# Performance work log

Hardware: AMD Instinct MI355X
Metric: run time of the kernel (lower is better)

Reference implementation:

```python
import jax, jax.numpy as jnp
import numpy as np

DIM = 256
HEADS = 4
DIM_HEAD = 32
HIDDEN = HEADS * DIM_HEAD  # 128
SCALE = DIM_HEAD ** -0.5
EPS = 1e-5


def setup_inputs() -> dict:
    key = jax.random.key(0)
    k1, k2, k3, k4 = jax.random.split(key, 4)
    B, D, H, W = 4, 32, 32, 32
    x = jax.random.normal(k1, (B, DIM, D, H, W), dtype=jnp.float32)
    # 1x1x1 convs are just channel-mixing matrices
    w_qkv = jax.random.normal(k2, (HIDDEN * 3, DIM), dtype=jnp.float32) * (DIM ** -0.5)
    w_out = jax.random.normal(k3, (DIM, HIDDEN), dtype=jnp.float32) * (HIDDEN ** -0.5)
    bias_out = jax.random.normal(k4, (DIM,), dtype=jnp.float32) * 0.02
    gamma = jnp.ones((DIM,), dtype=jnp.float32)
    beta = jnp.zeros((DIM,), dtype=jnp.float32)
    return {"x": x, "w_qkv": w_qkv, "w_out": w_out, "bias_out": bias_out,
            "gamma": gamma, "beta": beta}


def reference(x, w_qkv, w_out, bias_out, gamma, beta):
    B, C, D, H, W = x.shape
    n = D * H * W
    # to_qkv: 1x1x1 conv, no bias -> channel matmul
    qkv = jnp.einsum('oc,bcdhw->bodhw', w_qkv, x)  # [B, 3*HIDDEN, D, H, W]
    qkv = qkv.reshape(B, 3, HEADS, DIM_HEAD, n)
    q, k, v = qkv[:, 0], qkv[:, 1], qkv[:, 2]       # each [B, HEADS, DIM_HEAD, n]
    q = jax.nn.softmax(q, axis=-2) * SCALE          # softmax over head-dim channels
    k = jax.nn.softmax(k, axis=-1)                  # softmax over spatial positions
    context = jnp.einsum('bhdn,bhen->bhde', k, v)   # [B, H, dh, dh]
    out = jnp.einsum('bhde,bhdn->bhen', context, q) # [B, H, dh, n]
    out = out.reshape(B, HIDDEN, D, H, W)
    # to_out conv (1x1x1, with bias)
    y = jnp.einsum('oc,bcdhw->bodhw', w_out, out) + bias_out[None, :, None, None, None]
    # LayerNorm3D over channel dim
    mean = jnp.mean(y, axis=1, keepdims=True)
    var = jnp.var(y, axis=1, keepdims=True)
    y = (y - mean) / jnp.sqrt(var + EPS)
    return y * gamma[None, :, None, None, None] + beta[None, :, None, None, None]
```

## Files before the change

### kernel.cpp

```cpp
#include <hip/hip_runtime.h>


typedef unsigned short us16;
typedef __attribute__((ext_vector_type(8))) short short8v;
typedef __attribute__((ext_vector_type(4))) float f32x4;

#define B_ 4
#define C_ 256
#define NO_ 384
#define N_ 32768
#define HEADS_ 4
#define DH_ 32
#define HID_ 128
#define SCALE_ 0.17677669529663687f
#define EPS_ 1e-5f
#define NCHUNK 128
#define CHN 256

__device__ __forceinline__ float bf2f(us16 u) {
    union { unsigned int i; float f; } v; v.i = ((unsigned int)u) << 16; return v.f;
}
__device__ __forceinline__ us16 f2bf(float f) {
    union { float f; unsigned int i; } v; v.f = f;
    unsigned int x = v.i;
    return (us16)((x + 0x7fffu + ((x >> 16) & 1u)) >> 16);
}
__device__ __forceinline__ bool f32_mode(const void* gamma) {
    return *reinterpret_cast<const unsigned int*>(gamma) == 0x3F800000u;
}
__device__ __forceinline__ float ldin(const void* p, size_t i, bool m) {
    return m ? reinterpret_cast<const float*>(p)[i]
             : bf2f(reinterpret_cast<const us16*>(p)[i]);
}
__device__ __forceinline__ void gload_lds16(const us16* g, us16* l) {
    __builtin_amdgcn_global_load_lds(
        (__attribute__((address_space(1))) void*)g,
        (__attribute__((address_space(3))) void*)l, 16, 0, 0);
}

__global__ __launch_bounds__(256) void k_cvtw(
    const void* __restrict__ w, const void* __restrict__ gamma, us16* __restrict__ wb)
{
    const bool m32 = f32_mode(gamma);
    int i4 = (blockIdx.x * 256 + threadIdx.x) * 4;
    if (m32) {
        float4 f = *reinterpret_cast<const float4*>(reinterpret_cast<const float*>(w) + i4);
        ushort4 u; u.x = f2bf(f.x); u.y = f2bf(f.y); u.z = f2bf(f.z); u.w = f2bf(f.w);
        *reinterpret_cast<ushort4*>(wb + i4) = u;
    } else {
        *reinterpret_cast<ushort4*>(wb + i4) =
            *reinterpret_cast<const ushort4*>(reinterpret_cast<const us16*>(w) + i4);
    }
}

__global__ __launch_bounds__(256) void k_tr(
    const void* __restrict__ x, const void* __restrict__ gamma, us16* __restrict__ xt)
{
    __shared__ us16 T[64][72];
    const bool m32 = f32_mode(gamma);
    const int t = threadIdx.x;
    const int n0 = blockIdx.x * 64;
    const int c0 = blockIdx.y * 64;
    const int b  = blockIdx.z;

    const int cb = (t >> 4) * 4;
    const int nb = (t & 15) * 4;
    float v[4][4];
#pragma unroll
    for (int i = 0; i < 4; i++) {
        size_t off = ((size_t)b * C_ + c0 + cb + i) * N_ + n0 + nb;
        if (m32) {
            float4 f = *reinterpret_cast<const float4*>(reinterpret_cast<const float*>(x) + off);
            v[i][0] = f.x; v[i][1] = f.y; v[i][2] = f.z; v[i][3] = f.w;
        } else {
            ushort4 u = *reinterpret_cast<const ushort4*>(reinterpret_cast<const us16*>(x) + off);
            v[i][0] = bf2f(u.x); v[i][1] = bf2f(u.y); v[i][2] = bf2f(u.z); v[i][3] = bf2f(u.w);
        }
    }
#pragma unroll
    for (int j = 0; j < 4; j++) {
        ushort4 u;
        u.x = f2bf(v[0][j]); u.y = f2bf(v[1][j]); u.z = f2bf(v[2][j]); u.w = f2bf(v[3][j]);
        *reinterpret_cast<ushort4*>(&T[nb + j][cb]) = u;
    }
    __syncthreads();
    const int n = t >> 2;
    const int ch = (t & 3) * 16;
    uint4 r0 = *reinterpret_cast<const uint4*>(&T[n][ch]);
    uint4 r1 = *reinterpret_cast<const uint4*>(&T[n][ch + 8]);
    us16* dst = xt + ((size_t)b * N_ + n0 + n) * C_ + c0 + ch;
    *reinterpret_cast<uint4*>(dst)     = r0;
    *reinterpret_cast<uint4*>(dst + 8) = r1;
}

__global__ __launch_bounds__(256) void k_qkv(
    const us16* __restrict__ xt, const us16* __restrict__ wb, us16* __restrict__ qkv)
{
    __shared__ us16 As[128][64];
    __shared__ us16 Bs[128][64];
    const int t  = threadIdx.x;
    const int bb = blockIdx.z;
    const int o0 = blockIdx.y * 128;
    const int p0 = blockIdx.x * 128;
    const int wid  = t >> 6;
    const int lane = t & 63;
    const int lr   = lane & 15;
    const int quad = lane >> 4;
    const int m0w = (wid >> 1) * 64;
    const int n0w = (wid & 1) * 64;

    const int srow = wid * 32 + (lane >> 3);
    const int scol = ((lane & 7) ^ (lane >> 3)) * 8;

    f32x4 acc[4][4];
#pragma unroll
    for (int mi = 0; mi < 4; mi++)
#pragma unroll
        for (int nj = 0; nj < 4; nj++) acc[mi][nj] = (f32x4){0.f, 0.f, 0.f, 0.f};

    for (int c0 = 0; c0 < C_; c0 += 64) {
        const us16* ag = wb + (size_t)(o0 + srow) * C_ + c0 + scol;
        const us16* bg = xt + ((size_t)bb * N_ + p0 + srow) * C_ + c0 + scol;
        us16* al = &As[wid * 32][0];
        us16* bl = &Bs[wid * 32][0];
#pragma unroll
        for (int j = 0; j < 4; j++) {
            gload_lds16(ag + (size_t)j * 8 * C_, al + j * 512);
            gload_lds16(bg + (size_t)j * 8 * C_, bl + j * 512);
        }
        __syncthreads();
        const int sw = (lr & 7) << 3;
#pragma unroll
        for (int k32 = 0; k32 < 64; k32 += 32) {
            short8v a[4], bfr[4];
            const int col = (k32 + quad * 8) ^ sw;
#pragma unroll
            for (int mi = 0; mi < 4; mi++)
                a[mi] = *reinterpret_cast<const short8v*>(&As[m0w + mi * 16 + lr][col]);
#pragma unroll
            for (int nj = 0; nj < 4; nj++)
                bfr[nj] = *reinterpret_cast<const short8v*>(&Bs[n0w + nj * 16 + lr][col]);
#pragma unroll
            for (int mi = 0; mi < 4; mi++)
#pragma unroll
                for (int nj = 0; nj < 4; nj++)
                    acc[mi][nj] = __builtin_amdgcn_mfma_f32_16x16x32_bf16(
                        a[mi], bfr[nj], acc[mi][nj], 0, 0, 0);
        }
        __syncthreads();
    }
#pragma unroll
    for (int mi = 0; mi < 4; mi++) {
#pragma unroll
        for (int rr = 0; rr < 4; rr++) {
            int o = o0 + m0w + mi * 16 + quad * 4 + rr;
            us16* cp = qkv + ((size_t)bb * NO_ + o) * N_ + p0 + n0w + lr;
#pragma unroll
            for (int nj = 0; nj < 4; nj++)
                cp[nj * 16] = f2bf(acc[mi][nj][rr]);
        }
    }
}

__global__ __launch_bounds__(256) void k_ctx_part(
    const us16* __restrict__ qkv, float* __restrict__ part)
{
    __shared__ us16 Kp[32][264];
    __shared__ us16 Vt[32][264];
    __shared__ float redM[4][32];
    __shared__ float redS[4][32];
    const int t = threadIdx.x;
    const int chunk = blockIdx.x;
    const int h = blockIdx.y;
    const int b = blockIdx.z;
    const int p0 = chunk * CHN;
    const us16* kbase = qkv + ((size_t)b * NO_ + HID_ + h * DH_) * N_;
    const us16* vbase = qkv + ((size_t)b * NO_ + 2 * HID_ + h * DH_) * N_;

    {
        const int r = t >> 3, c = (t & 7) * 32;
        const us16* kp = kbase + (size_t)r * N_ + p0 + c;
        const us16* vp = vbase + (size_t)r * N_ + p0 + c;
#pragma unroll
        for (int j = 0; j < 4; j++) {
            *reinterpret_cast<uint4*>(&Kp[r][c + j * 8]) = *reinterpret_cast<const uint4*>(kp + j * 8);
            *reinterpret_cast<uint4*>(&Vt[r][c + j * 8]) = *reinterpret_cast<const uint4*>(vp + j * 8);
        }
    }
    __syncthreads();

    const int d    = t & 31;
    const int seg  = t >> 5;
    const int wv   = t >> 6;
    const int lane = t & 63;
    const int lr   = lane & 15;
    const int quad = lane >> 4;

    float kv[32];
#pragma unroll
    for (int j = 0; j < 4; j++) {
        uint4 kq = *reinterpret_cast<const uint4*>(&Kp[d][seg * 32 + j * 8]);
        const us16* ks = reinterpret_cast<const us16*>(&kq);
#pragma unroll
        for (int u = 0; u < 8; u++) kv[j * 8 + u] = bf2f(ks[u]);
    }
    float m = -1e30f;
#pragma unroll
    for (int u = 0; u < 32; u++) m = fmaxf(m, kv[u]);
    m = fmaxf(m, __shfl_xor(m, 32));
    if (lane < 32) redM[wv][d] = m;
    __syncthreads();
    m = fmaxf(fmaxf(redM[0][d], redM[1][d]), fmaxf(redM[2][d], redM[3][d]));

    float s = 0.f;
    us16 pb[32];
#pragma unroll
    for (int u = 0; u < 32; u++) {
        float pv = __expf(kv[u] - m);
        s += pv;
        pb[u] = f2bf(pv);
    }
#pragma unroll
    for (int j = 0; j < 4; j++)
        *reinterpret_cast<uint4*>(&Kp[d][seg * 32 + j * 8]) =
            *reinterpret_cast<const uint4*>(&pb[j * 8]);
    s += __shfl_xor(s, 32);
    if (lane < 32) redS[wv][d] = s;
    __syncthreads();

    f32x4 acc[2][2];
#pragma unroll
    for (int mi = 0; mi < 2; mi++)
#pragma unroll
        for (int nj = 0; nj < 2; nj++) acc[mi][nj] = (f32x4){0.f, 0.f, 0.f, 0.f};
#pragma unroll
    for (int kk = 0; kk < 64; kk += 32) {
        const int k32 = wv * 64 + kk;
        short8v a[2], bfr[2];
#pragma unroll
        for (int mi = 0; mi < 2; mi++)
            a[mi] = *reinterpret_cast<const short8v*>(&Kp[mi * 16 + lr][k32 + quad * 8]);
#pragma unroll
        for (int nj = 0; nj < 2; nj++)
            bfr[nj] = *reinterpret_cast<const short8v*>(&Vt[nj * 16 + lr][k32 + quad * 8]);
#pragma unroll
        for (int mi = 0; mi < 2; mi++)
#pragma unroll
            for (int nj = 0; nj < 2; nj++)
                acc[mi][nj] = __builtin_amdgcn_mfma_f32_16x16x32_bf16(
                    a[mi], bfr[nj], acc[mi][nj], 0, 0, 0);
    }
    __syncthreads();

    float* wpart = reinterpret_cast<float*>(&Kp[0][0]);
#pragma unroll
    for (int mi = 0; mi < 2; mi++)
#pragma unroll
        for (int nj = 0; nj < 2; nj++)
#pragma unroll
            for (int rr = 0; rr < 4; rr++)
                wpart[wv * 1056 + (mi * 16 + quad * 4 + rr) * 33 + nj * 16 + lr] =
                    acc[mi][nj][rr];
    __syncthreads();

    const size_t base = (((size_t)(b * HEADS_ + h)) * NCHUNK + chunk) * 1088;
    {
        const int dd = t >> 3, e4 = (t & 7) * 4;
        float o0 = 0.f, o1 = 0.f, o2 = 0.f, o3 = 0.f;
#pragma unroll
        for (int w = 0; w < 4; w++) {
            const float* wp = wpart + w * 1056 + dd * 33 + e4;
            o0 += wp[0]; o1 += wp[1]; o2 += wp[2]; o3 += wp[3];
        }
        *reinterpret_cast<float4*>(&part[base + 64 + dd * 32 + e4]) =
            make_float4(o0, o1, o2, o3);
    }
    if (t < 32) {
        part[base + t] = m;
        part[base + 32 + t] = redS[0][t] + redS[1][t] + redS[2][t] + redS[3][t];
    }
}

__global__ __launch_bounds__(1024) void k_ctx_comb(
    const float* __restrict__ part, float* __restrict__ ctx)
{
    __shared__ float scale[NCHUNK][32];
    __shared__ float Mg[32];
    __shared__ float Sg[32];
    __shared__ float redm[32][32];
    __shared__ float reds[32][32];
    const int t = threadIdx.x;
    const int bh = blockIdx.x;
    const float* pb = part + (size_t)bh * NCHUNK * 1088;

    const int d = t & 31, g = t >> 5;
    float m = -1e30f;
    for (int c = g; c < NCHUNK; c += 32) m = fmaxf(m, pb[(size_t)c * 1088 + d]);
    redm[g][d] = m;
    __syncthreads();
    if (t < 32) {
        float mm = redm[0][t];
#pragma unroll
        for (int w = 1; w < 32; w++) mm = fmaxf(mm, redm[w][t]);
        Mg[t] = mm;
    }
    __syncthreads();
    float sacc = 0.f;
    for (int c = g; c < NCHUNK; c += 32) {
        float sc = __expf(pb[(size_t)c * 1088 + d] - Mg[d]);
        scale[c][d] = sc;
        sacc += sc * pb[(size_t)c * 1088 + 32 + d];
    }
    reds[g][d] = sacc;
    __syncthreads();
    if (t < 32) {
        float ss = 0.f;
#pragma unroll
        for (int w = 0; w < 32; w++) ss += reds[w][t];
        Sg[t] = 1.f / ss;
    }
    __syncthreads();

    const int dd = t >> 5;
    const int e  = t & 31;
    float a = 0.f;
    for (int c = 0; c < NCHUNK; c++)
        a += scale[c][dd] * pb[(size_t)c * 1088 + 64 + dd * 32 + e];
    ctx[((size_t)bh * DH_ + dd) * DH_ + e] = a * Sg[dd];
}

__global__ __launch_bounds__(256) void k_ctx(
    const us16* __restrict__ qkv, float* __restrict__ ctx)
{
    const int d = blockIdx.x;
    const int h = blockIdx.y;
    const int b = blockIdx.z;
    const int tid = threadIdx.x;
    const us16* krow  = qkv + ((size_t)b * NO_ + HID_ + h * DH_ + d) * N_;
    const us16* vbase = qkv + ((size_t)b * NO_ + 2 * HID_ + h * DH_) * N_;
    __shared__ float red[4];
    __shared__ float part[4][DH_];

    float m = -1e30f;
    for (int i = tid; i < N_; i += 256) m = fmaxf(m, bf2f(krow[i]));
#pragma unroll
    for (int off = 32; off; off >>= 1) m = fmaxf(m, __shfl_xor(m, off));
    if ((tid & 63) == 0) red[tid >> 6] = m;
    __syncthreads();
    m = fmaxf(fmaxf(red[0], red[1]), fmaxf(red[2], red[3]));
    __syncthreads();
    float s = 0.f;
    for (int i = tid; i < N_; i += 256) s += __expf(bf2f(krow[i]) - m);
#pragma unroll
    for (int off = 32; off; off >>= 1) s += __shfl_xor(s, off);
    if ((tid & 63) == 0) red[tid >> 6] = s;
    __syncthreads();
    s = red[0] + red[1] + red[2] + red[3];
    const float inv = 1.f / s;

    float acc[DH_];
#pragma unroll
    for (int e = 0; e < DH_; e++) acc[e] = 0.f;
    for (int i = tid; i < N_; i += 256) {
        float p = __expf(bf2f(krow[i]) - m) * inv;
#pragma unroll
        for (int e = 0; e < DH_; e++) acc[e] += p * bf2f(vbase[(size_t)e * N_ + i]);
    }
#pragma unroll
    for (int e = 0; e < DH_; e++) {
        float v2 = acc[e];
#pragma unroll
        for (int off = 32; off; off >>= 1) v2 += __shfl_xor(v2, off);
        acc[e] = v2;
    }
    const int wid = tid >> 6;
    if ((tid & 63) == 0) {
#pragma unroll
        for (int e = 0; e < DH_; e++) part[wid][e] = acc[e];
    }
    __syncthreads();
    if (tid < DH_) {
        float v2 = part[0][tid] + part[1][tid] + part[2][tid] + part[3][tid];
        ctx[(((size_t)b * HEADS_ + h) * DH_ + d) * DH_ + tid] = v2;
    }
}

__global__ __launch_bounds__(256) void k_w2(
    const void* __restrict__ wout, const float* __restrict__ ctx,
    const void* __restrict__ gamma, us16* __restrict__ w2b)
{
    const bool m32 = f32_mode(gamma);
    const int b = blockIdx.y;
    const int gid = blockIdx.x * 256 + (int)threadIdx.x;
    const int i = gid & 127;
    const int o = gid >> 7;
    const int h = i >> 5, d = i & 31;
    const float* cr = ctx + (((size_t)b * HEADS_ + h) * DH_ + d) * DH_;
    const size_t woff = (size_t)o * HID_ + h * DH_;
    float s = 0.f;
#pragma unroll
    for (int e = 0; e < DH_; e++) s += ldin(wout, woff + e, m32) * cr[e];
    w2b[((size_t)b * C_ + o) * HID_ + i] = f2bf(s);
}

__global__ __launch_bounds__(256) void k_out(
    const us16* __restrict__ qkv, const us16* __restrict__ w2b,
    const void* __restrict__ bias, const void* __restrict__ gamma,
    const void* __restrict__ beta, void* __restrict__ y)
{
    __shared__ us16 qsT[64][136];
    __shared__ float red1[4][64];
    __shared__ float red2[4][64];
    __shared__ float meanS[64];
    __shared__ float rstdS[64];
    const bool m32 = f32_mode(gamma);
    const int t  = threadIdx.x;
    const int bb = blockIdx.y;
    const int p0 = blockIdx.x * 64;

    {
        const int h = t >> 6, col = t & 63;
        const us16* qb = qkv + ((size_t)bb * NO_ + h * DH_) * N_ + p0 + col;
        float ev[DH_];
        float mx = -1e30f;
#pragma unroll
        for (int d = 0; d < DH_; d++) { ev[d] = bf2f(qb[(size_t)d * N_]); mx = fmaxf(mx, ev[d]); }
        float ssum = 0.f;
#pragma unroll
        for (int d = 0; d < DH_; d++) { ev[d] = __expf(ev[d] - mx); ssum += ev[d]; }
        const float inv = SCALE_ / ssum;
#pragma unroll
        for (int d = 0; d < DH_; d += 2) {
            unsigned int pk = (unsigned int)f2bf(ev[d] * inv)
                            | ((unsigned int)f2bf(ev[d + 1] * inv) << 16);
            *reinterpret_cast<unsigned int*>(&qsT[col][h * DH_ + d]) = pk;
        }
    }
    __syncthreads();

    const int wid  = t >> 6;
    const int lane = t & 63;
    const int lr   = lane & 15;
    const int quad = lane >> 4;
    const int m0w  = wid * 64;
    const us16* w2bb = w2b + (size_t)bb * C_ * HID_;

    float bv[4][4];
#pragma unroll
    for (int mi = 0; mi < 4; mi++)
#pragma unroll
        for (int rr = 0; rr < 4; rr++)
            bv[mi][rr] = ldin(bias, m0w + mi * 16 + quad * 4 + rr, m32);

    f32x4 acc[4][4];
#pragma unroll
    for (int mi = 0; mi < 4; mi++)
#pragma unroll
        for (int nj = 0; nj < 4; nj++) {
            f32x4 c;
#pragma unroll
            for (int rr = 0; rr < 4; rr++) c[rr] = bv[mi][rr];
            acc[mi][nj] = c;
        }

#pragma unroll
    for (int ks = 0; ks < HID_; ks += 32) {
        short8v a[4], bfr[4];
#pragma unroll
        for (int mi = 0; mi < 4; mi++)
            a[mi] = *reinterpret_cast<const short8v*>(
                w2bb + (size_t)(m0w + mi * 16 + lr) * HID_ + ks + quad * 8);
#pragma unroll
        for (int nj = 0; nj < 4; nj++)
            bfr[nj] = *reinterpret_cast<const short8v*>(&qsT[nj * 16 + lr][ks + quad * 8]);
#pragma unroll
        for (int mi = 0; mi < 4; mi++)
#pragma unroll
            for (int nj = 0; nj < 4; nj++)
                acc[mi][nj] = __builtin_amdgcn_mfma_f32_16x16x32_bf16(
                    a[mi], bfr[nj], acc[mi][nj], 0, 0, 0);
    }

#pragma unroll
    for (int nj = 0; nj < 4; nj++) {
        float s1 = 0.f, s2 = 0.f;
#pragma unroll
        for (int mi = 0; mi < 4; mi++)
#pragma unroll
            for (int rr = 0; rr < 4; rr++) {
                float vv = acc[mi][nj][rr];
                s1 += vv; s2 += vv * vv;
            }
        s1 += __shfl_xor(s1, 16); s2 += __shfl_xor(s2, 16);
        s1 += __shfl_xor(s1, 32); s2 += __shfl_xor(s2, 32);
        if (quad == 0) { red1[wid][nj * 16 + lr] = s1; red2[wid][nj * 16 + lr] = s2; }
    }
    __syncthreads();
    if (t < 64) {
        float s1 = red1[0][t] + red1[1][t] + red1[2][t] + red1[3][t];
        float s2 = red2[0][t] + red2[1][t] + red2[2][t] + red2[3][t];
        float mean = s1 * (1.f / C_);
        float var = s2 * (1.f / C_) - mean * mean;
        meanS[t] = mean;
        rstdS[t] = rsqrtf(var + EPS_);
    }
    __syncthreads();

#pragma unroll
    for (int mi = 0; mi < 4; mi++) {
#pragma unroll
        for (int rr = 0; rr < 4; rr++) {
            const int o = m0w + mi * 16 + quad * 4 + rr;
            const float g  = ldin(gamma, o, m32);
            const float be = ldin(beta, o, m32);
            if (m32) {
                float* yp = reinterpret_cast<float*>(y) + ((size_t)bb * C_ + o) * N_ + p0 + lr;
#pragma unroll
                for (int nj = 0; nj < 4; nj++) {
                    int col = nj * 16 + lr;
                    yp[nj * 16] = (acc[mi][nj][rr] - meanS[col]) * rstdS[col] * g + be;
                }
            } else {
                us16* yp = reinterpret_cast<us16*>(y) + ((size_t)bb * C_ + o) * N_ + p0 + lr;
#pragma unroll
                for (int nj = 0; nj < 4; nj++) {
                    int col = nj * 16 + lr;
                    yp[nj * 16] = f2bf((acc[mi][nj][rr] - meanS[col]) * rstdS[col] * g + be);
                }
            }
        }
    }
}

#define K1_BM 128
#define K1_BN 128
#define K1_BK 32
__global__ __launch_bounds__(256, 2) void k_qkv_simt(
    const void* __restrict__ x, const void* __restrict__ w,
    const void* __restrict__ gamma, us16* __restrict__ qkv)
{
    __shared__ float Wt[K1_BK][K1_BM];
    __shared__ float Xs[K1_BK][K1_BN];
    const bool m32 = f32_mode(gamma);
    const int tid = threadIdx.x;
    const int b  = blockIdx.z;
    const int o0 = blockIdx.y * K1_BM;
    const int p0 = blockIdx.x * K1_BN;
    const int tx = tid & 15;
    const int ty = tid >> 4;

    float acc[8][8];
#pragma unroll
    for (int i = 0; i < 8; i++)
#pragma unroll
        for (int j = 0; j < 8; j++) acc[i][j] = 0.f;

    for (int c0 = 0; c0 < C_; c0 += K1_BK) {
#pragma unroll
        for (int rep = 0; rep < 2; rep++) {
            int i = rep * 2048 + tid * 8;
            int r = i >> 5;
            int c = i & 31;
            size_t off = (size_t)(o0 + r) * C_ + c0 + c;
            if (m32) {
                const float* wp = reinterpret_cast<const float*>(w) + off;
                float4 f0 = *reinterpret_cast<const float4*>(wp);
                float4 f1 = *reinterpret_cast<const float4*>(wp + 4);
                Wt[c + 0][r] = f0.x; Wt[c + 1][r] = f0.y;
                Wt[c + 2][r] = f0.z; Wt[c + 3][r] = f0.w;
                Wt[c + 4][r] = f1.x; Wt[c + 5][r] = f1.y;
                Wt[c + 6][r] = f1.z; Wt[c + 7][r] = f1.w;
            } else {
                union { uint4 v; us16 s[8]; } u;
                u.v = *reinterpret_cast<const uint4*>(reinterpret_cast<const us16*>(w) + off);
#pragma unroll
                for (int j = 0; j < 8; j++) Wt[c + j][r] = bf2f(u.s[j]);
            }
        }
#pragma unroll
        for (int rep = 0; rep < 2; rep++) {
            int i = rep * 2048 + tid * 8;
            int r = i >> 7;
            int c = i & 127;
            size_t off = (size_t)b * C_ * N_ + (size_t)(c0 + r) * N_ + p0 + c;
            if (m32) {
                const float* xp = reinterpret_cast<const float*>(x) + off;
                float4 f0 = *reinterpret_cast<const float4*>(xp);
                float4 f1 = *reinterpret_cast<const float4*>(xp + 4);
                Xs[r][c + 0] = f0.x; Xs[r][c + 1] = f0.y;
                Xs[r][c + 2] = f0.z; Xs[r][c + 3] = f0.w;
                Xs[r][c + 4] = f1.x; Xs[r][c + 5] = f1.y;
                Xs[r][c + 6] = f1.z; Xs[r][c + 7] = f1.w;
            } else {
                union { uint4 v; us16 s[8]; } u;
                u.v = *reinterpret_cast<const uint4*>(reinterpret_cast<const us16*>(x) + off);
#pragma unroll
                for (int j = 0; j < 8; j++) Xs[r][c + j] = bf2f(u.s[j]);
            }
        }
        __syncthreads();
#pragma unroll 8
        for (int kk = 0; kk < K1_BK; kk++) {
            float a[8], xv[8];
            float4 a0 = *reinterpret_cast<const float4*>(&Wt[kk][ty * 8]);
            float4 a1 = *reinterpret_cast<const float4*>(&Wt[kk][ty * 8 + 4]);
            a[0] = a0.x; a[1] = a0.y; a[2] = a0.z; a[3] = a0.w;
            a[4] = a1.x; a[5] = a1.y; a[6] = a1.z; a[7] = a1.w;
#pragma unroll
            for (int j = 0; j < 8; j++) xv[j] = Xs[kk][tx + 16 * j];
#pragma unroll
            for (int i = 0; i < 8; i++)
#pragma unroll
                for (int j = 0; j < 8; j++) acc[i][j] += a[i] * xv[j];
        }
        __syncthreads();
    }
    us16* cp = qkv + ((size_t)b * NO_ + o0) * N_ + p0;
#pragma unroll
    for (int i = 0; i < 8; i++) {
#pragma unroll
        for (int j = 0; j < 8; j++)
            cp[(size_t)(ty * 8 + i) * N_ + tx + 16 * j] = f2bf(acc[i][j]);
    }
}

extern "C" void kernel_launch(void* const* d_in, const int* in_sizes, int n_in,
                              void* d_out, int out_size, void* d_ws, size_t ws_size,
                              hipStream_t stream) {
    (void)in_sizes; (void)n_in; (void)out_size;
    const void* x      = d_in[0];
    const void* w_qkv  = d_in[1];
    const void* w_out  = d_in[2];
    const void* bias   = d_in[3];
    const void* gamma  = d_in[4];
    const void* beta   = d_in[5];

    char* ws = (char*)d_ws;
    const size_t QKV_OFF = 0;
    const size_t XT_OFF  = 100663296;
    const size_t BIG_CTX = 167772160;
    const size_t BIG_WB  = 167837696;
    const size_t BIG_W2  = 168034304;
    const size_t BIG_END = 168296448;

    us16* qkv = (us16*)(ws + QKV_OFF);
    const bool big = ws_size >= BIG_END;

    float* ctx;
    us16*  w2b;
    if (big) {
        us16*  xt   = (us16*)(ws + XT_OFF);
        float* prt  = (float*)(ws + XT_OFF);
        us16*  wbf  = (us16*)(ws + BIG_WB);
        ctx = (float*)(ws + BIG_CTX);
        w2b = (us16*)(ws + BIG_W2);
        k_cvtw<<<dim3(96), 256, 0, stream>>>(w_qkv, gamma, wbf);
        k_tr  <<<dim3(N_ / 64, C_ / 64, B_), 256, 0, stream>>>(x, gamma, xt);
        k_qkv <<<dim3(N_ / 128, NO_ / 128, B_), 256, 0, stream>>>(xt, wbf, qkv);
        k_ctx_part<<<dim3(NCHUNK, HEADS_, B_), 256, 0, stream>>>(qkv, prt);
        k_ctx_comb<<<dim3(B_ * HEADS_), 1024, 0, stream>>>(prt, ctx);
    } else {
        ctx = (float*)(ws + 100663296);
        w2b = (us16*)(ws + 100663296 + 65536);
        k_qkv_simt<<<dim3(N_ / 128, NO_ / 128, B_), 256, 0, stream>>>(x, w_qkv, gamma, qkv);
        k_ctx<<<dim3(DH_, HEADS_, B_), 256, 0, stream>>>(qkv, ctx);
    }
    k_w2 <<<dim3(128, B_), 256, 0, stream>>>(w_out, ctx, gamma, w2b);
    k_out<<<dim3(N_ / 64, B_), 256, 0, stream>>>(qkv, w2b, bias, gamma, beta, d_out);
}
```

Before: 349.0 us.

## Fuse input transpose into QKV GEMM by loading x directly into LDS

Removes the separate transpose kernel that wrote a bf16 channel-last copy of x. The QKV GEMM now reads x directly in its native channel-major layout, converts it to bf16 in registers and writes the transposed tile into padded LDS. The grid is also reordered so the three output-channel tiles for the same spatial tile are adjacent and can share x through cache. This saves a full write and re-read of the intermediate tensor. In exchange, the B operand is now loaded with scalar per-element global reads rather than async 16-byte direct-to-LDS loads, so that load can no longer overlap the same way.

```diff
diff --git a/kernel.cpp b/kernel.cpp
--- a/kernel.cpp
+++ b/kernel.cpp
@@ -53,55 +53,17 @@
     }
 }
 
-__global__ __launch_bounds__(256) void k_tr(
-    const void* __restrict__ x, const void* __restrict__ gamma, us16* __restrict__ xt)
-{
-    __shared__ us16 T[64][72];
+__global__ __launch_bounds__(256) void k_qkv(
+    const void* __restrict__ x, const us16* __restrict__ wb,
+    const void* __restrict__ gamma, us16* __restrict__ qkv)
+{
+    __shared__ us16 As[128][64];
+    __shared__ us16 Bs[128][72];
     const bool m32 = f32_mode(gamma);
-    const int t = threadIdx.x;
-    const int n0 = blockIdx.x * 64;
-    const int c0 = blockIdx.y * 64;
-    const int b  = blockIdx.z;
-
-    const int cb = (t >> 4) * 4;
-    const int nb = (t & 15) * 4;
-    float v[4][4];
-#pragma unroll
-    for (int i = 0; i < 4; i++) {
-        size_t off = ((size_t)b * C_ + c0 + cb + i) * N_ + n0 + nb;
-        if (m32) {
-            float4 f = *reinterpret_cast<const float4*>(reinterpret_cast<const float*>(x) + off);
-            v[i][0] = f.x; v[i][1] = f.y; v[i][2] = f.z; v[i][3] = f.w;
-        } else {
-            ushort4 u = *reinterpret_cast<const ushort4*>(reinterpret_cast<const us16*>(x) + off);
-            v[i][0] = bf2f(u.x); v[i][1] = bf2f(u.y); v[i][2] = bf2f(u.z); v[i][3] = bf2f(u.w);
-        }
-    }
-#pragma unroll
-    for (int j = 0; j < 4; j++) {
-        ushort4 u;
-        u.x = f2bf(v[0][j]); u.y = f2bf(v[1][j]); u.z = f2bf(v[2][j]); u.w = f2bf(v[3][j]);
-        *reinterpret_cast<ushort4*>(&T[nb + j][cb]) = u;
-    }
-    __syncthreads();
-    const int n = t >> 2;
-    const int ch = (t & 3) * 16;
-    uint4 r0 = *reinterpret_cast<const uint4*>(&T[n][ch]);
-    uint4 r1 = *reinterpret_cast<const uint4*>(&T[n][ch + 8]);
-    us16* dst = xt + ((size_t)b * N_ + n0 + n) * C_ + c0 + ch;
-    *reinterpret_cast<uint4*>(dst)     = r0;
-    *reinterpret_cast<uint4*>(dst + 8) = r1;
-}
-
-__global__ __launch_bounds__(256) void k_qkv(
-    const us16* __restrict__ xt, const us16* __restrict__ wb, us16* __restrict__ qkv)
-{
-    __shared__ us16 As[128][64];
-    __shared__ us16 Bs[128][64];
     const int t  = threadIdx.x;
     const int bb = blockIdx.z;
-    const int o0 = blockIdx.y * 128;
-    const int p0 = blockIdx.x * 128;
+    const int o0 = blockIdx.x * 128;
+    const int p0 = blockIdx.y * 128;
     const int wid  = t >> 6;
     const int lane = t & 63;
     const int lr   = lane & 15;
@@ -112,6 +74,9 @@
     const int srow = wid * 32 + (lane >> 3);
     const int scol = ((lane & 7) ^ (lane >> 3)) * 8;
 
+    const int l  = t & 31;
+    const int cb = (t >> 5) * 8;
+
     f32x4 acc[4][4];
 #pragma unroll
     for (int mi = 0; mi < 4; mi++)
@@ -120,26 +85,53 @@
 
     for (int c0 = 0; c0 < C_; c0 += 64) {
         const us16* ag = wb + (size_t)(o0 + srow) * C_ + c0 + scol;
-        const us16* bg = xt + ((size_t)bb * N_ + p0 + srow) * C_ + c0 + scol;
         us16* al = &As[wid * 32][0];
-        us16* bl = &Bs[wid * 32][0];
-#pragma unroll
-        for (int j = 0; j < 4; j++) {
+#pragma unroll
+        for (int j = 0; j < 4; j++)
             gload_lds16(ag + (size_t)j * 8 * C_, al + j * 512);
-            gload_lds16(bg + (size_t)j * 8 * C_, bl + j * 512);
+
+        {
+            us16 bfv[8][4];
+            if (m32) {
+                const float* xp = reinterpret_cast<const float*>(x)
+                                + ((size_t)bb * C_ + c0 + cb) * N_ + p0 + l;
+#pragma unroll
+                for (int j = 0; j < 8; j++)
+#pragma unroll
+                    for (int k = 0; k < 4; k++)
+                        bfv[j][k] = f2bf(xp[(size_t)j * N_ + k * 32]);
+            } else {
+                const us16* xp = reinterpret_cast<const us16*>(x)
+                               + ((size_t)bb * C_ + c0 + cb) * N_ + p0 + l;
+#pragma unroll
+                for (int j = 0; j < 8; j++)
+#pragma unroll
+                    for (int k = 0; k < 4; k++)
+                        bfv[j][k] = xp[(size_t)j * N_ + k * 32];
+            }
+#pragma unroll
+            for (int k = 0; k < 4; k++) {
+                us16 pk[8];
+#pragma unroll
+                for (int j = 0; j < 8; j++) pk[j] = bfv[j][k];
+                *reinterpret_cast<uint4*>(&Bs[l + 32 * k][cb]) =
+                    *reinterpret_cast<const uint4*>(pk);
+            }
         }
         __syncthreads();
+
         const int sw = (lr & 7) << 3;
 #pragma unroll
         for (int k32 = 0; k32 < 64; k32 += 32) {
             short8v a[4], bfr[4];
-            const int col = (k32 + quad * 8) ^ sw;
+            const int colA = (k32 + quad * 8) ^ sw;
 #pragma unroll
             for (int mi = 0; mi < 4; mi++)
-                a[mi] = *reinterpret_cast<const short8v*>(&As[m0w + mi * 16 + lr][col]);
+                a[mi] = *reinterpret_cast<const short8v*>(&As[m0w + mi * 16 + lr][colA]);
 #pragma unroll
             for (int nj = 0; nj < 4; nj++)
-                bfr[nj] = *reinterpret_cast<const short8v*>(&Bs[n0w + nj * 16 + lr][col]);
+                bfr[nj] = *reinterpret_cast<const short8v*>(
+                    &Bs[n0w + nj * 16 + lr][k32 + quad * 8]);
 #pragma unroll
             for (int mi = 0; mi < 4; mi++)
 #pragma unroll
@@ -649,14 +641,12 @@
     float* ctx;
     us16*  w2b;
     if (big) {
-        us16*  xt   = (us16*)(ws + XT_OFF);
         float* prt  = (float*)(ws + XT_OFF);
         us16*  wbf  = (us16*)(ws + BIG_WB);
         ctx = (float*)(ws + BIG_CTX);
         w2b = (us16*)(ws + BIG_W2);
         k_cvtw<<<dim3(96), 256, 0, stream>>>(w_qkv, gamma, wbf);
-        k_tr  <<<dim3(N_ / 64, C_ / 64, B_), 256, 0, stream>>>(x, gamma, xt);
-        k_qkv <<<dim3(N_ / 128, NO_ / 128, B_), 256, 0, stream>>>(xt, wbf, qkv);
+        k_qkv <<<dim3(NO_ / 128, N_ / 128, B_), 256, 0, stream>>>(x, wbf, gamma, qkv);
         k_ctx_part<<<dim3(NCHUNK, HEADS_, B_), 256, 0, stream>>>(qkv, prt);
         k_ctx_comb<<<dim3(B_ * HEADS_), 1024, 0, stream>>>(prt, ctx);
     } else {
```

New measurement: 333.6 us. -4.4%, faster.
